# Performance work log

Hardware: AMD Instinct MI355X
Metric: run time of the kernel (lower is better)

Reference implementation:

```python
import jax, jax.numpy as jnp
import numpy as np

T, K, E, H, I = 1024, 2, 8, 2048, 1024


def setup_inputs() -> dict:
    key = jax.random.key(0)
    k1, k2, k3, k4 = jax.random.split(key, 4)
    hidden_states = jax.random.normal(k1, (T, H), dtype=jnp.float32)
    selected_experts = jax.random.randint(k2, (T, K), 0, E, dtype=jnp.int32)
    # glorot-ish scale for the batched expert kernels
    gu_scale = (2.0 / (H + 2 * I)) ** 0.5
    dn_scale = (2.0 / (I + H)) ** 0.5
    gate_up_proj = jax.random.normal(k3, (E, 2 * I, H), dtype=jnp.float32) * gu_scale
    down_proj = jax.random.normal(k4, (E, H, I), dtype=jnp.float32) * dn_scale
    return {
        "hidden_states": hidden_states,
        "selected_experts": selected_experts,
        "gate_up_proj": gate_up_proj,
        "down_proj": down_proj,
    }


def reference(hidden_states, selected_experts, gate_up_proj, down_proj):
    # Mathematically identical to the original per-token weight gather
    # (ops.take + 'th,temh->tem'), but expressed as dense all-expert GEMMs
    # followed by an output gather, avoiding the T*k*2I*H weight blowup.
    # gate_up_all: (T, E, 2I)
    gate_up_all = jnp.einsum("th,emh->tem", hidden_states, gate_up_proj)
    gate, up = jnp.split(gate_up_all, 2, axis=-1)
    intermediate = jax.nn.silu(gate) * up                # (T, E, I)
    out_all = jnp.einsum("tem,ehm->teh", intermediate, down_proj)  # (T, E, H)
    # select the top-k experts' outputs per token -> (T, K, H)
    return jnp.take_along_axis(out_all, selected_experts[..., None].astype(jnp.int32), axis=1)
```

## Files before the change

kernel.cpp:

```cpp
#include <hip/hip_runtime.h>
#include <hip/hip_bf16.h>

#define T_TOK 1024
#define KSEL  2
#define NEXP  8
#define HDIM  2048
#define IDIM  1024
#define TK    2048

#define BR 72
#define MT 3

typedef float  f32x4  __attribute__((ext_vector_type(4)));
typedef __bf16 bf16x8 __attribute__((ext_vector_type(8)));
typedef __bf16 bf16x2 __attribute__((ext_vector_type(2)));

__device__ __forceinline__ unsigned short f2bf(float f) {
    union { float f; unsigned u; } v; v.f = f;
    unsigned r = (v.u >> 16) & 1u;
    return (unsigned short)((v.u + 0x7fffu + r) >> 16);
}

__device__ __forceinline__ unsigned pk2bf(float lo, float hi) {
#if __has_builtin(__builtin_amdgcn_cvt_pk_bf16_f32)
    bf16x2 v = __builtin_amdgcn_cvt_pk_bf16_f32(lo, hi);
    union { bf16x2 v; unsigned u; } c; c.v = v;
    return c.u;
#else
    return (unsigned)f2bf(lo) | ((unsigned)f2bf(hi) << 16);
#endif
}

__device__ __forceinline__ void wg_barrier_nodrain() {
    asm volatile("s_waitcnt lgkmcnt(0)" ::: "memory");
    __builtin_amdgcn_s_barrier();
}

__global__ __launch_bounds__(256) void prep(
    const float* __restrict__ hidden, const int* __restrict__ sel,
    unsigned short* __restrict__ hid_bf, int* __restrict__ meta,
    int* __restrict__ pairs)
{
    const int t = blockIdx.x * 256 + threadIdx.x;
    {
        const float* s = hidden + (size_t)t * 8;
        float4 v0 = *(const float4*)s;
        float4 v1 = *(const float4*)(s + 4);
        uint4 o;
        o.x = pk2bf(v0.x, v0.y); o.y = pk2bf(v0.z, v0.w);
        o.z = pk2bf(v1.x, v1.y); o.w = pk2bf(v1.z, v1.w);
        *(uint4*)(hid_bf + (size_t)t * 8) = o;
    }
    if (blockIdx.x == 0) {
        __shared__ int lcnt[NEXP], lstart[NEXP], lfill[NEXP];
        const int tid = threadIdx.x;
        if (tid < NEXP) { lcnt[tid] = 0; lfill[tid] = 0; }
        __syncthreads();
        for (int i = tid; i < TK; i += 256) atomicAdd(&lcnt[sel[i]], 1);
        __syncthreads();
        if (tid == 0) {
            int s2 = 0;
            for (int e2 = 0; e2 < NEXP; ++e2) { lstart[e2] = s2; s2 += lcnt[e2]; }
        }
        __syncthreads();
        for (int i = tid; i < TK; i += 256) {
            int e2 = sel[i];
            pairs[lstart[e2] + atomicAdd(&lfill[e2], 1)] = i;
        }
        if (tid < NEXP) { meta[tid] = lcnt[tid]; meta[NEXP + tid] = lstart[tid]; }
    }
}

__global__ __launch_bounds__(512, 2) void gemm1_gateup(
    const unsigned short* __restrict__ hid_bf, const float* __restrict__ gup,
    const int* __restrict__ meta, const int* __restrict__ pairs,
    unsigned short* __restrict__ inter)
{
    __shared__ __align__(16) unsigned short Bs[3][64 * BR];

    const int bx = blockIdx.x;
    const int e = bx & 7, nt = (bx >> 3) & 31, mt = bx >> 8;
    const int cnt = meta[e];
    const int m0 = mt * 384;
    if (m0 >= cnt) return;
    const int seg  = meta[8 + e];
    const int rows = cnt - m0;
    const int n0   = nt * 32;

    const int tid  = threadIdx.x;
    const int lane = tid & 63, w = tid >> 6;
    const int quad = lane >> 4, l16 = lane & 15;

    const int brow = tid >> 3, bkc = (tid & 7) * 8;
    const int grow = (brow < 32) ? (n0 + brow) : (IDIM + n0 + (brow - 32));
    const float* __restrict__ bp =
        gup + (size_t)e * (2 * IDIM * HDIM) + (size_t)grow * HDIM + bkc;
    const int bofs = brow * BR + bkc;

    const unsigned short* ap[3];
    #pragma unroll
    for (int i = 0; i < 3; ++i) {
        int mr  = m0 + w * 48 + i * 16 + l16;
        int idx = seg + min(mr, cnt - 1);
        ap[i] = hid_bf + (size_t)(pairs[idx] >> 1) * HDIM + quad * 8;
    }

    f32x4 accg[3][2], accu[3][2];
    const f32x4 zero = {0.f, 0.f, 0.f, 0.f};
    #pragma unroll
    for (int i = 0; i < 3; ++i)
        #pragma unroll
        for (int j = 0; j < 2; ++j) { accg[i][j] = zero; accu[i][j] = zero; }

    float4 Br0[2], Br1[2];
    bf16x8 afA[3][2], afB[3][2];

    auto loadB = [&](float4 (&br)[2], int s) {
        const float* p = bp + s * 64;
        br[0] = *(const float4*)p;
        br[1] = *(const float4*)(p + 4);
    };
    auto storeB = [&](const float4 (&br)[2], int buf) {
        uint4 o;
        o.x = pk2bf(br[0].x, br[0].y); o.y = pk2bf(br[0].z, br[0].w);
        o.z = pk2bf(br[1].x, br[1].y); o.w = pk2bf(br[1].z, br[1].w);
        *(uint4*)&Bs[buf][bofs] = o;
    };
    auto loadA = [&](bf16x8 (&af)[3][2], int s) {
        #pragma unroll
        for (int i = 0; i < 3; ++i)
            #pragma unroll
            for (int kk = 0; kk < 2; ++kk)
                af[i][kk] = *(const bf16x8*)(ap[i] + s * 64 + kk * 32);
    };
    auto compute = [&](const bf16x8 (&af)[3][2], int buf) {
        #pragma unroll
        for (int kk = 0; kk < 2; ++kk) {
            const int ko = kk * 32 + quad * 8;
            bf16x8 bg[2], bu[2];
            #pragma unroll
            for (int j = 0; j < 2; ++j) {
                bg[j] = *(const bf16x8*)&Bs[buf][(j * 16 + l16) * BR + ko];
                bu[j] = *(const bf16x8*)&Bs[buf][(32 + j * 16 + l16) * BR + ko];
            }
            #pragma unroll
            for (int i = 0; i < 3; ++i)
                #pragma unroll
                for (int j = 0; j < 2; ++j) {
                    accg[i][j] = __builtin_amdgcn_mfma_f32_16x16x32_bf16(af[i][kk], bg[j], accg[i][j], 0, 0, 0);
                    accu[i][j] = __builtin_amdgcn_mfma_f32_16x16x32_bf16(af[i][kk], bu[j], accu[i][j], 0, 0, 0);
                }
        }
    };

    const int NK = HDIM / 64;
    loadB(Br0, 0);
    loadA(afA, 0);
    storeB(Br0, 0);
    loadB(Br0, 1);
    loadB(Br1, 2);
    wg_barrier_nodrain();

    for (int s = 0; s < NK; s += 2) {
        storeB(Br0, (s + 1) % 3);
        if (s + 3 < NK) loadB(Br0, s + 3);
        loadA(afB, s + 1);
        compute(afA, s % 3);
        wg_barrier_nodrain();
        if (s + 2 < NK) storeB(Br1, (s + 2) % 3);
        if (s + 4 < NK) loadB(Br1, s + 4);
        if (s + 2 < NK) loadA(afA, s + 2);
        compute(afB, (s + 1) % 3);
        wg_barrier_nodrain();
    }

    #pragma unroll
    for (int i = 0; i < 3; ++i) {
        #pragma unroll
        for (int r = 0; r < 4; ++r) {
            int mrow = w * 48 + i * 16 + quad * 4 + r;
            if (mrow < rows && mrow < 384) {
                size_t orow = (size_t)(seg + m0 + mrow) * IDIM;
                #pragma unroll
                for (int j = 0; j < 2; ++j) {
                    float g = accg[i][j][r], u = accu[i][j][r];
                    float sv = g * (1.f / (1.f + __expf(-g)));
                    inter[orow + n0 + j * 16 + l16] = f2bf(sv * u);
                }
            }
        }
    }
}

__global__ __launch_bounds__(512, 2) void gemm2_down(
    const unsigned short* __restrict__ inter, const float* __restrict__ down,
    const int* __restrict__ meta, const int* __restrict__ pairs,
    float* __restrict__ out)
{
    __shared__ __align__(16) unsigned short Bs[3][64 * BR];

    const int bx = blockIdx.x;
    const int e = bx & 7, nt = (bx >> 3) & 31, mt = bx >> 8;
    const int cnt = meta[e];
    const int m0 = mt * 384;
    if (m0 >= cnt) return;
    const int seg  = meta[8 + e];
    const int rows = cnt - m0;
    const int n0   = nt * 64;

    const int tid  = threadIdx.x;
    const int lane = tid & 63, w = tid >> 6;
    const int quad = lane >> 4, l16 = lane & 15;

    const int brow = tid >> 3, bkc = (tid & 7) * 8;
    const float* __restrict__ bp =
        down + (size_t)e * (HDIM * IDIM) + (size_t)(n0 + brow) * IDIM + bkc;
    const int bofs = brow * BR + bkc;

    const unsigned short* ap[3];
    #pragma unroll
    for (int i = 0; i < 3; ++i) {
        int mr  = m0 + w * 48 + i * 16 + l16;
        int idx = seg + min(mr, cnt - 1);
        ap[i] = inter + (size_t)idx * IDIM + quad * 8;
    }

    f32x4 acc[3][4];
    const f32x4 zero = {0.f, 0.f, 0.f, 0.f};
    #pragma unroll
    for (int i = 0; i < 3; ++i)
        #pragma unroll
        for (int j = 0; j < 4; ++j) acc[i][j] = zero;

    float4 Br0[2], Br1[2];
    bf16x8 afA[3][2], afB[3][2];

    auto loadB = [&](float4 (&br)[2], int s) {
        const float* p = bp + s * 64;
        br[0] = *(const float4*)p;
        br[1] = *(const float4*)(p + 4);
    };
    auto storeB = [&](const float4 (&br)[2], int buf) {
        uint4 o;
        o.x = pk2bf(br[0].x, br[0].y); o.y = pk2bf(br[0].z, br[0].w);
        o.z = pk2bf(br[1].x, br[1].y); o.w = pk2bf(br[1].z, br[1].w);
        *(uint4*)&Bs[buf][bofs] = o;
    };
    auto loadA = [&](bf16x8 (&af)[3][2], int s) {
        #pragma unroll
        for (int i = 0; i < 3; ++i)
            #pragma unroll
            for (int kk = 0; kk < 2; ++kk)
                af[i][kk] = *(const bf16x8*)(ap[i] + s * 64 + kk * 32);
    };
    auto compute = [&](const bf16x8 (&af)[3][2], int buf) {
        #pragma unroll
        for (int kk = 0; kk < 2; ++kk) {
            const int ko = kk * 32 + quad * 8;
            bf16x8 bf[4];
            #pragma unroll
            for (int j = 0; j < 4; ++j)
                bf[j] = *(const bf16x8*)&Bs[buf][(j * 16 + l16) * BR + ko];
            #pragma unroll
            for (int i = 0; i < 3; ++i)
                #pragma unroll
                for (int j = 0; j < 4; ++j)
                    acc[i][j] = __builtin_amdgcn_mfma_f32_16x16x32_bf16(af[i][kk], bf[j], acc[i][j], 0, 0, 0);
        }
    };

    const int NK = IDIM / 64;
    loadB(Br0, 0);
    loadA(afA, 0);
    storeB(Br0, 0);
    loadB(Br0, 1);
    loadB(Br1, 2);
    wg_barrier_nodrain();

    for (int s = 0; s < NK; s += 2) {
        storeB(Br0, (s + 1) % 3);
        if (s + 3 < NK) loadB(Br0, s + 3);
        loadA(afB, s + 1);
        compute(afA, s % 3);
        wg_barrier_nodrain();
        if (s + 2 < NK) storeB(Br1, (s + 2) % 3);
        if (s + 4 < NK) loadB(Br1, s + 4);
        if (s + 2 < NK) loadA(afA, s + 2);
        compute(afB, (s + 1) % 3);
        wg_barrier_nodrain();
    }

    #pragma unroll
    for (int i = 0; i < 3; ++i) {
        #pragma unroll
        for (int r = 0; r < 4; ++r) {
            int mrow = w * 48 + i * 16 + quad * 4 + r;
            if (mrow < rows && mrow < 384) {
                int p = pairs[seg + m0 + mrow];
                size_t ob = (size_t)p * HDIM + n0 + l16;
                #pragma unroll
                for (int j = 0; j < 4; ++j)
                    out[ob + j * 16] = acc[i][j][r];
            }
        }
    }
}

extern "C" void kernel_launch(void* const* d_in, const int* in_sizes, int n_in,
                              void* d_out, int out_size, void* d_ws, size_t ws_size,
                              hipStream_t stream) {
    const float* hidden = (const float*)d_in[0];
    const int*   sel    = (const int*)  d_in[1];
    const float* gup    = (const float*)d_in[2];
    const float* down   = (const float*)d_in[3];
    float* out = (float*)d_out;

    char* ws = (char*)d_ws;
    int* meta  = (int*)ws;
    int* pairs = meta + 16;
    unsigned short* inter  = (unsigned short*)(ws + 16384);
    unsigned short* hid_bf = inter + (size_t)TK * IDIM;

    prep<<<T_TOK * HDIM / 8 / 256, 256, 0, stream>>>(hidden, sel, hid_bf, meta, pairs);
    gemm1_gateup<<<MT * 32 * 8, 512, 0, stream>>>(hid_bf, gup, meta, pairs, inter);
    gemm2_down  <<<MT * 32 * 8, 512, 0, stream>>>(inter, down, meta, pairs, out);
}
```

Baseline: 290.3 us.

## Deepen weight-tile pipeline to four LDS stages and skip idle waves' compute

Both expert GEMM kernels move from a three-buffer, two-step software pipeline to a four-buffer, four-step unrolled pipeline. Weight loads from global memory are now issued four K-steps ahead, which keeps more float loads in flight to hide latency. Waves whose 48-row slice lies entirely past the expert's token count now skip their A-fragment loads and MFMA compute, while still taking part in weight staging and barriers. The cost is more LDS per block and more registers for the extra weight prefetch buffers, which could lower occupancy under launch_bounds(512,2).

New measurement: 293.7 us. No clear change (+1.2%).

```diff
diff --git a/kernel.cpp b/kernel.cpp
--- a/kernel.cpp
+++ b/kernel.cpp
@@ -76,7 +76,7 @@
     const int* __restrict__ meta, const int* __restrict__ pairs,
     unsigned short* __restrict__ inter)
 {
-    __shared__ __align__(16) unsigned short Bs[3][64 * BR];
+    __shared__ __align__(16) unsigned short Bs[4][64 * BR];
 
     const int bx = blockIdx.x;
     const int e = bx & 7, nt = (bx >> 3) & 31, mt = bx >> 8;
@@ -90,6 +90,7 @@
     const int tid  = threadIdx.x;
     const int lane = tid & 63, w = tid >> 6;
     const int quad = lane >> 4, l16 = lane & 15;
+    const bool wact = (w * 48) < rows;
 
     const int brow = tid >> 3, bkc = (tid & 7) * 8;
     const int grow = (brow < 32) ? (n0 + brow) : (IDIM + n0 + (brow - 32));
@@ -112,8 +113,8 @@
         #pragma unroll
         for (int j = 0; j < 2; ++j) { accg[i][j] = zero; accu[i][j] = zero; }
 
-    float4 Br0[2], Br1[2];
-    bf16x8 afA[3][2], afB[3][2];
+    float4 Br0_[2], Br1_[2], Br2_[2], Br3_[2];
+    bf16x8 afX[3][2], afY[3][2];
 
     auto loadB = [&](float4 (&br)[2], int s) {
         const float* p = bp + s * 64;
@@ -154,23 +155,35 @@
     };
 
     const int NK = HDIM / 64;
-    loadB(Br0, 0);
-    loadA(afA, 0);
-    storeB(Br0, 0);
-    loadB(Br0, 1);
-    loadB(Br1, 2);
+    loadB(Br0_, 0);
+    if (wact) loadA(afX, 0);
+    storeB(Br0_, 0);
+    loadB(Br1_, 1);
+    loadB(Br2_, 2);
+    loadB(Br3_, 3);
+    loadB(Br0_, 4);
     wg_barrier_nodrain();
 
-    for (int s = 0; s < NK; s += 2) {
-        storeB(Br0, (s + 1) % 3);
-        if (s + 3 < NK) loadB(Br0, s + 3);
-        loadA(afB, s + 1);
-        compute(afA, s % 3);
-        wg_barrier_nodrain();
-        if (s + 2 < NK) storeB(Br1, (s + 2) % 3);
-        if (s + 4 < NK) loadB(Br1, s + 4);
-        if (s + 2 < NK) loadA(afA, s + 2);
-        compute(afB, (s + 1) % 3);
+    for (int s = 0; s < NK; s += 4) {
+        if (wact) loadA(afY, s + 1);
+        storeB(Br1_, 1);
+        if (s + 5 < NK) loadB(Br1_, s + 5);
+        if (wact) compute(afX, 0);
+        wg_barrier_nodrain();
+        if (wact) loadA(afX, s + 2);
+        storeB(Br2_, 2);
+        if (s + 6 < NK) loadB(Br2_, s + 6);
+        if (wact) compute(afY, 1);
+        wg_barrier_nodrain();
+        if (wact) loadA(afY, s + 3);
+        storeB(Br3_, 3);
+        if (s + 7 < NK) loadB(Br3_, s + 7);
+        if (wact) compute(afX, 2);
+        wg_barrier_nodrain();
+        if (wact && s + 4 < NK) loadA(afX, s + 4);
+        if (s + 4 < NK) storeB(Br0_, 0);
+        if (s + 8 < NK) loadB(Br0_, s + 8);
+        if (wact) compute(afY, 3);
         wg_barrier_nodrain();
     }
 
@@ -197,7 +210,7 @@
     const int* __restrict__ meta, const int* __restrict__ pairs,
     float* __restrict__ out)
 {
-    __shared__ __align__(16) unsigned short Bs[3][64 * BR];
+    __shared__ __align__(16) unsigned short Bs[4][64 * BR];
 
     const int bx = blockIdx.x;
     const int e = bx & 7, nt = (bx >> 3) & 31, mt = bx >> 8;
@@ -211,6 +224,7 @@
     const int tid  = threadIdx.x;
     const int lane = tid & 63, w = tid >> 6;
     const int quad = lane >> 4, l16 = lane & 15;
+    const bool wact = (w * 48) < rows;
 
     const int brow = tid >> 3, bkc = (tid & 7) * 8;
     const float* __restrict__ bp =
@@ -232,8 +246,8 @@
         #pragma unroll
         for (int j = 0; j < 4; ++j) acc[i][j] = zero;
 
-    float4 Br0[2], Br1[2];
-    bf16x8 afA[3][2], afB[3][2];
+    float4 Br0_[2], Br1_[2], Br2_[2], Br3_[2];
+    bf16x8 afX[3][2], afY[3][2];
 
     auto loadB = [&](float4 (&br)[2], int s) {
         const float* p = bp + s * 64;
@@ -270,23 +284,38 @@
     };
 
     const int NK = IDIM / 64;
-    loadB(Br0, 0);
-    loadA(afA, 0);
-    storeB(Br0, 0);
-    loadB(Br0, 1);
-    loadB(Br1, 2);
+    loadB(Br0_, 0);
+    if (wact) loadA(afX, 0);
+    storeB(Br0_, 0);
+    loadB(Br1_, 1);
+    loadB(Br2_, 2);
+    loadB(Br3_, 3);
+    loadB(Br0_, 4);
     wg_barrier_nodrain();
 
-    for (int s = 0; s < NK; s += 2) {
-        storeB(Br0, (s + 1) % 3);
-        if (s + 3 < NK) loadB(Br0, s + 3);
-        loadA(afB, s + 1);
-        compute(afA, s % 3);
-        wg_barrier_nodrain();
-        if (s + 2 < NK) storeB(Br1, (s + 2) % 3);
-        if (s + 4 < NK) loadB(Br1, s + 4);
-        if (s + 2 < NK) loadA(afA, s + 2);
-        compute(afB, (s + 1) % 3);
+    for (int s = 0; s < NK; s += 4) {
+        if (wact) loadA(afY, s + 1);
+        storeB(Br1_, 1);
+        if (s + 5 < NK) loadB(Br1_, s + 5);
+        if (wact) compute(afX, 0);
+        wg_barrier_nodrain();
+
+        if (wact) loadA(afX, s + 2);
+        storeB(Br2_, 2);
+        if (s + 6 < NK) loadB(Br2_, s + 6);
+        if (wact) compute(afY, 1);
+        wg_barrier_nodrain();
+
+        if (wact) loadA(afY, s + 3);
+        storeB(Br3_, 3);
+        if (s + 7 < NK) loadB(Br3_, s + 7);
+        if (wact) compute(afX, 2);
+        wg_barrier_nodrain();
+
+        if (wact && s + 4 < NK) loadA(afX, s + 4);
+        if (s + 4 < NK) storeB(Br0_, 0);
+        if (s + 8 < NK) loadB(Br0_, s + 8);
+        if (wact) compute(afY, 3);
         wg_barrier_nodrain();
     }
 
```

## Halve M-tile to 192 rows with 256-thread blocks, skip idle waves, stagger K start

Applied to the files above, without the earlier changes.

Both grouped GEMMs now use 256-thread blocks covering 192 token rows instead of 512 threads covering 384. The grid doubles to six M-tiles per expert so the uneven per-expert counts are split more finely. Each thread now loads 16 fp32 weights per stage instead of 8, and waves whose rows are all past the expert count skip their A loads and MFMAs. A per-block phase rotates the K-loop starting point so that blocks in flight read different K slices of the weight rows at the same time. The trade-off is that each fp32 weight tile is re-read by twice as many M-blocks, which adds weight traffic.

Measured after the change: 399.4 us. 37.6% more time.

```diff
diff --git a/kernel.cpp b/kernel.cpp
--- a/kernel.cpp
+++ b/kernel.cpp
@@ -9,7 +9,7 @@
 #define TK    2048
 
 #define BR 72
-#define MT 3
+#define MT2 6
 
 typedef float  f32x4  __attribute__((ext_vector_type(4)));
 typedef __bf16 bf16x8 __attribute__((ext_vector_type(8)));
@@ -71,7 +71,7 @@
     }
 }
 
-__global__ __launch_bounds__(512, 2) void gemm1_gateup(
+__global__ __launch_bounds__(256, 3) void gemm1_gateup(
     const unsigned short* __restrict__ hid_bf, const float* __restrict__ gup,
     const int* __restrict__ meta, const int* __restrict__ pairs,
     unsigned short* __restrict__ inter)
@@ -81,7 +81,7 @@
     const int bx = blockIdx.x;
     const int e = bx & 7, nt = (bx >> 3) & 31, mt = bx >> 8;
     const int cnt = meta[e];
-    const int m0 = mt * 384;
+    const int m0 = mt * 192;
     if (m0 >= cnt) return;
     const int seg  = meta[8 + e];
     const int rows = cnt - m0;
@@ -90,8 +90,13 @@
     const int tid  = threadIdx.x;
     const int lane = tid & 63, w = tid >> 6;
     const int quad = lane >> 4, l16 = lane & 15;
-
-    const int brow = tid >> 3, bkc = (tid & 7) * 8;
+    const bool wact = (w * 48) < rows;
+
+    const int NK  = HDIM / 64;
+    const int NKM = NK - 1;
+    const int phase = (nt + e) & NKM;
+
+    const int brow = tid >> 2, bkc = (tid & 3) * 16;
     const int grow = (brow < 32) ? (n0 + brow) : (IDIM + n0 + (brow - 32));
     const float* __restrict__ bp =
         gup + (size_t)e * (2 * IDIM * HDIM) + (size_t)grow * HDIM + bkc;
@@ -112,26 +117,32 @@
         #pragma unroll
         for (int j = 0; j < 2; ++j) { accg[i][j] = zero; accu[i][j] = zero; }
 
-    float4 Br0[2], Br1[2];
+    float4 Br0[4], Br1[4];
     bf16x8 afA[3][2], afB[3][2];
 
-    auto loadB = [&](float4 (&br)[2], int s) {
-        const float* p = bp + s * 64;
+    auto loadB = [&](float4 (&br)[4], int s) {
+        const float* p = bp + ((s + phase) & NKM) * 64;
         br[0] = *(const float4*)p;
         br[1] = *(const float4*)(p + 4);
-    };
-    auto storeB = [&](const float4 (&br)[2], int buf) {
-        uint4 o;
-        o.x = pk2bf(br[0].x, br[0].y); o.y = pk2bf(br[0].z, br[0].w);
-        o.z = pk2bf(br[1].x, br[1].y); o.w = pk2bf(br[1].z, br[1].w);
-        *(uint4*)&Bs[buf][bofs] = o;
+        br[2] = *(const float4*)(p + 8);
+        br[3] = *(const float4*)(p + 12);
+    };
+    auto storeB = [&](const float4 (&br)[4], int buf) {
+        uint4 o0, o1;
+        o0.x = pk2bf(br[0].x, br[0].y); o0.y = pk2bf(br[0].z, br[0].w);
+        o0.z = pk2bf(br[1].x, br[1].y); o0.w = pk2bf(br[1].z, br[1].w);
+        o1.x = pk2bf(br[2].x, br[2].y); o1.y = pk2bf(br[2].z, br[2].w);
+        o1.z = pk2bf(br[3].x, br[3].y); o1.w = pk2bf(br[3].z, br[3].w);
+        *(uint4*)&Bs[buf][bofs]     = o0;
+        *(uint4*)&Bs[buf][bofs + 8] = o1;
     };
     auto loadA = [&](bf16x8 (&af)[3][2], int s) {
+        const int so = ((s + phase) & NKM) * 64;
         #pragma unroll
         for (int i = 0; i < 3; ++i)
             #pragma unroll
             for (int kk = 0; kk < 2; ++kk)
-                af[i][kk] = *(const bf16x8*)(ap[i] + s * 64 + kk * 32);
+                af[i][kk] = *(const bf16x8*)(ap[i] + so + kk * 32);
     };
     auto compute = [&](const bf16x8 (&af)[3][2], int buf) {
         #pragma unroll
@@ -153,9 +164,8 @@
         }
     };
 
-    const int NK = HDIM / 64;
     loadB(Br0, 0);
-    loadA(afA, 0);
+    if (wact) loadA(afA, 0);
     storeB(Br0, 0);
     loadB(Br0, 1);
     loadB(Br1, 2);
@@ -164,13 +174,13 @@
     for (int s = 0; s < NK; s += 2) {
         storeB(Br0, (s + 1) % 3);
         if (s + 3 < NK) loadB(Br0, s + 3);
-        loadA(afB, s + 1);
-        compute(afA, s % 3);
+        if (wact) loadA(afB, s + 1);
+        if (wact) compute(afA, s % 3);
         wg_barrier_nodrain();
         if (s + 2 < NK) storeB(Br1, (s + 2) % 3);
         if (s + 4 < NK) loadB(Br1, s + 4);
-        if (s + 2 < NK) loadA(afA, s + 2);
-        compute(afB, (s + 1) % 3);
+        if (wact && s + 2 < NK) loadA(afA, s + 2);
+        if (wact) compute(afB, (s + 1) % 3);
         wg_barrier_nodrain();
     }
 
@@ -179,7 +189,7 @@
         #pragma unroll
         for (int r = 0; r < 4; ++r) {
             int mrow = w * 48 + i * 16 + quad * 4 + r;
-            if (mrow < rows && mrow < 384) {
+            if (mrow < rows && mrow < 192) {
                 size_t orow = (size_t)(seg + m0 + mrow) * IDIM;
                 #pragma unroll
                 for (int j = 0; j < 2; ++j) {
@@ -192,7 +202,7 @@
     }
 }
 
-__global__ __launch_bounds__(512, 2) void gemm2_down(
+__global__ __launch_bounds__(256, 3) void gemm2_down(
     const unsigned short* __restrict__ inter, const float* __restrict__ down,
     const int* __restrict__ meta, const int* __restrict__ pairs,
     float* __restrict__ out)
@@ -202,7 +212,7 @@
     const int bx = blockIdx.x;
     const int e = bx & 7, nt = (bx >> 3) & 31, mt = bx >> 8;
     const int cnt = meta[e];
-    const int m0 = mt * 384;
+    const int m0 = mt * 192;
     if (m0 >= cnt) return;
     const int seg  = meta[8 + e];
     const int rows = cnt - m0;
@@ -211,8 +221,13 @@
     const int tid  = threadIdx.x;
     const int lane = tid & 63, w = tid >> 6;
     const int quad = lane >> 4, l16 = lane & 15;
-
-    const int brow = tid >> 3, bkc = (tid & 7) * 8;
+    const bool wact = (w * 48) < rows;
+
+    const int NK  = IDIM / 64;
+    const int NKM = NK - 1;
+    const int phase = (nt + e) & NKM;
+
+    const int brow = tid >> 2, bkc = (tid & 3) * 16;
     const float* __restrict__ bp =
         down + (size_t)e * (HDIM * IDIM) + (size_t)(n0 + brow) * IDIM + bkc;
     const int bofs = brow * BR + bkc;
@@ -232,26 +247,32 @@
         #pragma unroll
         for (int j = 0; j < 4; ++j) acc[i][j] = zero;
 
-    float4 Br0[2], Br1[2];
+    float4 Br0[4], Br1[4];
     bf16x8 afA[3][2], afB[3][2];
 
-    auto loadB = [&](float4 (&br)[2], int s) {
-        const float* p = bp + s * 64;
+    auto loadB = [&](float4 (&br)[4], int s) {
+        const float* p = bp + ((s + phase) & NKM) * 64;
         br[0] = *(const float4*)p;
         br[1] = *(const float4*)(p + 4);
-    };
-    auto storeB = [&](const float4 (&br)[2], int buf) {
-        uint4 o;
-        o.x = pk2bf(br[0].x, br[0].y); o.y = pk2bf(br[0].z, br[0].w);
-        o.z = pk2bf(br[1].x, br[1].y); o.w = pk2bf(br[1].z, br[1].w);
-        *(uint4*)&Bs[buf][bofs] = o;
+        br[2] = *(const float4*)(p + 8);
+        br[3] = *(const float4*)(p + 12);
+    };
+    auto storeB = [&](const float4 (&br)[4], int buf) {
+        uint4 o0, o1;
+        o0.x = pk2bf(br[0].x, br[0].y); o0.y = pk2bf(br[0].z, br[0].w);
+        o0.z = pk2bf(br[1].x, br[1].y); o0.w = pk2bf(br[1].z, br[1].w);
+        o1.x = pk2bf(br[2].x, br[2].y); o1.y = pk2bf(br[2].z, br[2].w);
+        o1.z = pk2bf(br[3].x, br[3].y); o1.w = pk2bf(br[3].z, br[3].w);
+        *(uint4*)&Bs[buf][bofs]     = o0;
+        *(uint4*)&Bs[buf][bofs + 8] = o1;
     };
     auto loadA = [&](bf16x8 (&af)[3][2], int s) {
+        const int so = ((s + phase) & NKM) * 64;
         #pragma unroll
         for (int i = 0; i < 3; ++i)
             #pragma unroll
             for (int kk = 0; kk < 2; ++kk)
-                af[i][kk] = *(const bf16x8*)(ap[i] + s * 64 + kk * 32);
+                af[i][kk] = *(const bf16x8*)(ap[i] + so + kk * 32);
     };
     auto compute = [&](const bf16x8 (&af)[3][2], int buf) {
         #pragma unroll
@@ -269,9 +290,8 @@
         }
     };
 
-    const int NK = IDIM / 64;
     loadB(Br0, 0);
-    loadA(afA, 0);
+    if (wact) loadA(afA, 0);
     storeB(Br0, 0);
     loadB(Br0, 1);
     loadB(Br1, 2);
@@ -280,13 +300,13 @@
     for (int s = 0; s < NK; s += 2) {
         storeB(Br0, (s + 1) % 3);
         if (s + 3 < NK) loadB(Br0, s + 3);
-        loadA(afB, s + 1);
-        compute(afA, s % 3);
+        if (wact) loadA(afB, s + 1);
+        if (wact) compute(afA, s % 3);
         wg_barrier_nodrain();
         if (s + 2 < NK) storeB(Br1, (s + 2) % 3);
         if (s + 4 < NK) loadB(Br1, s + 4);
-        if (s + 2 < NK) loadA(afA, s + 2);
-        compute(afB, (s + 1) % 3);
+        if (wact && s + 2 < NK) loadA(afA, s + 2);
+        if (wact) compute(afB, (s + 1) % 3);
         wg_barrier_nodrain();
     }
 
@@ -295,7 +315,7 @@
         #pragma unroll
         for (int r = 0; r < 4; ++r) {
             int mrow = w * 48 + i * 16 + quad * 4 + r;
-            if (mrow < rows && mrow < 384) {
+            if (mrow < rows && mrow < 192) {
                 int p = pairs[seg + m0 + mrow];
                 size_t ob = (size_t)p * HDIM + n0 + l16;
                 #pragma unroll
@@ -322,6 +342,6 @@
     unsigned short* hid_bf = inter + (size_t)TK * IDIM;
 
     prep<<<T_TOK * HDIM / 8 / 256, 256, 0, stream>>>(hidden, sel, hid_bf, meta, pairs);
-    gemm1_gateup<<<MT * 32 * 8, 512, 0, stream>>>(hid_bf, gup, meta, pairs, inter);
-    gemm2_down  <<<MT * 32 * 8, 512, 0, stream>>>(inter, down, meta, pairs, out);
-}
+    gemm1_gateup<<<MT2 * 32 * 8, 256, 0, stream>>>(hid_bf, gup, meta, pairs, inter);
+    gemm2_down  <<<MT2 * 32 * 8, 256, 0, stream>>>(inter, down, meta, pairs, out);
+}
```
